# Kernel optimization log

Hardware: AMD Instinct MI355X
Metric: run time of the kernel (lower is better)

The kernel has to match this reference:

```python
import jax, jax.numpy as jnp
import numpy as np

LABEL_SIZE = 64
START = LABEL_SIZE - 2
STOP = LABEL_SIZE - 1
NEG = -10000.0


def setup_inputs() -> dict:
    key = jax.random.key(0)
    k1, k2 = jax.random.split(key)
    B, T, L = 512, 512, LABEL_SIZE
    emissions = jax.random.normal(k1, (B, T, L), dtype=jnp.float32)
    # xavier-uniform-ish init, then mask row START (nothing transitions INTO start
    # ... actually transitions[next, prev]: row START = transitions into START)
    bound = float(np.sqrt(6.0 / (L + L)))
    trans = jax.random.uniform(k2, (L, L), dtype=jnp.float32, minval=-bound, maxval=bound)
    trans = trans.at[START, :].set(NEG)   # never transition to START
    trans = trans.at[:, STOP].set(NEG)    # never transition from STOP
    return {"input": emissions, "transitions": trans}


def reference(input, transitions):
    # input: [B, T, L] emission scores; transitions[next_tag, prev_tag]: [L, L]
    B, T, L = input.shape
    init = jnp.full((B, L), NEG, dtype=input.dtype).at[:, START].set(0.0)

    def step(forward_var, emit_t):
        # forward_var: [B, L] (over prev tag); emit_t: [B, L] (over next tag)
        # scores[b, next, prev] = forward_var[b, prev] + transitions[next, prev]
        nv = jax.nn.logsumexp(forward_var[:, None, :] + transitions[None, :, :], axis=-1)
        return nv + emit_t, None

    forward_var, _ = jax.lax.scan(step, init, jnp.swapaxes(input, 0, 1))  # scan over T
    terminal = forward_var + transitions[STOP][None, :]
    return jax.nn.logsumexp(terminal, axis=-1)  # [B] log partition function
```

## Files before the change

### kernel.cpp

```cpp
#include <hip/hip_runtime.h>
#include <hip/hip_bf16.h>

#define NTAG 64
#define TLEN 512
#define START_TAG 62
#define STOP_TAG 63
#define CHUNK 32
#define HALF (TLEN / 2)

#if __has_builtin(__builtin_amdgcn_fdot2_f32_bf16)
#define USE_DOT2 1
typedef __attribute__((ext_vector_type(2))) __bf16 bfv2;
typedef __attribute__((ext_vector_type(8))) __bf16 bfv8;
#endif

__device__ __forceinline__ unsigned short f2bfu(float f) {
    __hip_bfloat16 h = __float2bfloat16(f);
    unsigned short u; __builtin_memcpy(&u, &h, 2); return u;
}
#ifdef USE_DOT2
__device__ __forceinline__ __bf16 f2bf(float f) {
    unsigned short u = f2bfu(f); __bf16 b; __builtin_memcpy(&b, &u, 2); return b;
}
#endif

__global__ __launch_bounds__(128) void crf_fwd_bwd(
    const float* __restrict__ emis,
    const float* __restrict__ trans,
    float* __restrict__ out)
{
    const int b    = blockIdx.x;
    const int tid  = threadIdx.x;
    const int lane = tid & 63;
    const int w    = tid >> 6;

    __shared__ float lds[2 * 2 * CHUNK * NTAG];
#ifdef USE_DOT2
    __shared__ __align__(16) unsigned short xbf[2][NTAG];
    unsigned short* xs = xbf[w];
#else
    __shared__ __align__(16) float xf32[2][NTAG];
    float* xs = xf32[w];
#endif
    __shared__ float shv[2][NTAG];

    const float L2E = 1.4426950408889634f;
    const float LN2 = 0.6931471805599453f;

#ifdef USE_DOT2
    bfv2 Epk[NTAG / 2];
    #pragma unroll
    for (int k2 = 0; k2 < NTAG / 2; ++k2) {
        float e0, e1;
        if (w == 0) {
            e0 = exp2f(trans[lane * NTAG + 2 * k2]     * L2E);
            e1 = exp2f(trans[lane * NTAG + 2 * k2 + 1] * L2E);
        } else {
            e0 = exp2f(trans[(2 * k2) * NTAG + lane]     * L2E);
            e1 = exp2f(trans[(2 * k2 + 1) * NTAG + lane] * L2E);
        }
        bfv2 p; p[0] = f2bf(e0); p[1] = f2bf(e1);
        Epk[k2] = p;
    }
#else
    float E[NTAG];
    #pragma unroll
    for (int k = 0; k < NTAG; ++k)
        E[k] = exp2f(((w == 0) ? trans[lane * NTAG + k]
                               : trans[k * NTAG + lane]) * L2E);
#endif

    const float* eb = emis + (size_t)b * TLEN * NTAG;

    float4 r0, r1, r2, r3, r4, r5, r6, r7;
    #define LOAD_CHUNK(baseT)                                        \
        do {                                                         \
            const float4* gp = (const float4*)(eb + (baseT) * NTAG); \
            r0 = gp[0 * 64 + lane]; r1 = gp[1 * 64 + lane];          \
            r2 = gp[2 * 64 + lane]; r3 = gp[3 * 64 + lane];          \
            r4 = gp[4 * 64 + lane]; r5 = gp[5 * 64 + lane];          \
            r6 = gp[6 * 64 + lane]; r7 = gp[7 * 64 + lane];          \
        } while (0)
    #define EXP4(v) make_float4(exp2f((v).x * L2E), exp2f((v).y * L2E), \
                                exp2f((v).z * L2E), exp2f((v).w * L2E))
    #define STORE_CHUNK_EXP(bufp)                                    \
        do {                                                         \
            float4* b4 = (float4*)(bufp);                            \
            b4[0 * 64 + lane] = EXP4(r0); b4[1 * 64 + lane] = EXP4(r1); \
            b4[2 * 64 + lane] = EXP4(r2); b4[3 * 64 + lane] = EXP4(r3); \
            b4[4 * 64 + lane] = EXP4(r4); b4[5 * 64 + lane] = EXP4(r5); \
            b4[6 * 64 + lane] = EXP4(r6); b4[7 * 64 + lane] = EXP4(r7); \
        } while (0)

#ifdef USE_DOT2
    #define PAIR(X, i) __builtin_shufflevector(X, X, 2 * (i), 2 * (i) + 1)
    #define DOTQ(acc, X, base)                                                     \
        acc = __builtin_amdgcn_fdot2_f32_bf16(Epk[(base) + 0], PAIR(X, 0), acc, false); \
        acc = __builtin_amdgcn_fdot2_f32_bf16(Epk[(base) + 1], PAIR(X, 1), acc, false); \
        acc = __builtin_amdgcn_fdot2_f32_bf16(Epk[(base) + 2], PAIR(X, 2), acc, false); \
        acc = __builtin_amdgcn_fdot2_f32_bf16(Epk[(base) + 3], PAIR(X, 3), acc, false);
    #define MATVEC_REF(ssum, e_)                                     \
        do {                                                         \
            const bfv8* xq_ = (const bfv8*)xs;                       \
            bfv8 X0 = xq_[0], X1 = xq_[1], X2 = xq_[2], X3 = xq_[3]; \
            bfv8 X4 = xq_[4], X5 = xq_[5], X6 = xq_[6], X7 = xq_[7]; \
            unsigned short ru_;                                      \
            { __bf16 rb_ = X0[0]; __builtin_memcpy(&ru_, &rb_, 2); } \
            int ef_ = (int)((ru_ >> 7) & 0xffu);                     \
            e_ = (ef_ == 0) ? 0 : ef_ - 127;                         \
            float a0 = 0.f, a1 = 0.f, a2 = 0.f, a3 = 0.f;            \
            DOTQ(a0, X0, 0)  DOTQ(a1, X1, 4)                         \
            DOTQ(a2, X2, 8)  DOTQ(a3, X3, 12)                        \
            DOTQ(a0, X4, 16) DOTQ(a1, X5, 20)                        \
            DOTQ(a2, X6, 24) DOTQ(a3, X7, 28)                        \
            ssum = (a0 + a1) + (a2 + a3);                            \
        } while (0)
    #define WRITE_STATE(v) (xs[lane] = f2bfu(v))
#else
    #define MATVEC_REF(ssum, e_)                                     \
        do {                                                         \
            const float4* xq_ = (const float4*)xs;                   \
            float4 xv_[16];                                          \
            _Pragma("unroll")                                        \
            for (int j = 0; j < 16; ++j) xv_[j] = xq_[j];            \
            int ef_ = (int)((__float_as_uint(xv_[0].x) >> 23) & 0xffu); \
            e_ = (ef_ == 0) ? 0 : ef_ - 127;                         \
            float a0=0.f,a1=0.f,a2=0.f,a3=0.f;                       \
            float a4=0.f,a5=0.f,a6=0.f,a7=0.f;                       \
            _Pragma("unroll")                                        \
            for (int j = 0; j < 16; j += 2) {                        \
                a0 = fmaf(xv_[j].x,     E[4*j + 0], a0);             \
                a1 = fmaf(xv_[j].y,     E[4*j + 1], a1);             \
                a2 = fmaf(xv_[j].z,     E[4*j + 2], a2);             \
                a3 = fmaf(xv_[j].w,     E[4*j + 3], a3);             \
                a4 = fmaf(xv_[j + 1].x, E[4*j + 4], a4);             \
                a5 = fmaf(xv_[j + 1].y, E[4*j + 5], a5);             \
                a6 = fmaf(xv_[j + 1].z, E[4*j + 6], a6);             \
                a7 = fmaf(xv_[j + 1].w, E[4*j + 7], a7);             \
            }                                                        \
            ssum = ((a0 + a1) + (a2 + a3)) + ((a4 + a5) + (a6 + a7)); \
        } while (0)
    #define WRITE_STATE(v) (xs[lane] = (v))
#endif

    #define STEP(buf, s)                                             \
        do {                                                         \
            float em_ = (buf)[(s) * NTAG + lane];                    \
            float ssum_; int e_;                                     \
            MATVEC_REF(ssum_, e_);                                   \
            off += e_;                                               \
            float rs_ = __uint_as_float((unsigned)(127 - e_) << 23); \
            x = ssum_ * em_ * rs_;                                   \
            WRITE_STATE(x);                                          \
        } while (0)

    float x = 0.0f;
    int   off = 0;

    if (w == 0) {
        WRITE_STATE(lane == START_TAG ? 1.0f : 0.0f);

        LOAD_CHUNK(0);
        #pragma clang loop unroll(disable)
        for (int ci = 0; ci < 8; ++ci) {
            float* buf = &lds[(ci & 1) * (CHUNK * NTAG)];
            STORE_CHUNK_EXP(buf);
            if (ci < 7) LOAD_CHUNK((ci + 1) * CHUNK);

            #pragma clang loop unroll_count(4)
            for (int s = 0; s < CHUNK; ++s) STEP(buf, s);
        }
    } else {
        float Sv = exp2f(trans[STOP_TAG * NTAG + lane] * L2E);

        LOAD_CHUNK(HALF + 7 * CHUNK);
        #pragma clang loop unroll(disable)
        for (int i = 0; i < 8; ++i) {
            float* buf = &lds[(2 + (i & 1)) * (CHUNK * NTAG)];
            STORE_CHUNK_EXP(buf);
            if (i < 7) LOAD_CHUNK(HALF + (6 - i) * CHUNK);

            int s0 = CHUNK - 1;
            if (i == 0) {
                WRITE_STATE(Sv * buf[(CHUNK - 1) * NTAG + lane]);
                s0 = CHUNK - 2;
            }
            #pragma clang loop unroll_count(4)
            for (int s = s0; s >= 0; --s) STEP(buf, s);
        }
        {
            float ssum_; int e_;
            MATVEC_REF(ssum_, e_);
            off += e_;
            x = ssum_ * __uint_as_float((unsigned)(127 - e_) << 23);
        }
    }

    shv[w][lane] = log2f(x) + (float)off;
    __syncthreads();

    if (w == 0) {
        float v = shv[0][lane] + shv[1][lane];
        float m = v;
        #pragma unroll
        for (int d = 1; d < 64; d <<= 1) m = fmaxf(m, __shfl_xor(m, d, 64));
        float e = exp2f(v - m);
        #pragma unroll
        for (int d = 1; d < 64; d <<= 1) e += __shfl_xor(e, d, 64);
        if (lane == 0) out[b] = LN2 * (m + log2f(e));
    }
}

extern "C" void kernel_launch(void* const* d_in, const int* in_sizes, int n_in,
                              void* d_out, int out_size, void* d_ws, size_t ws_size,
                              hipStream_t stream) {
    const float* emis  = (const float*)d_in[0];
    const float* trans = (const float*)d_in[1];
    float* out = (float*)d_out;
    (void)in_sizes; (void)n_in; (void)out_size; (void)d_ws; (void)ws_size;
    crf_fwd_bwd<<<512, 128, 0, stream>>>(emis, trans, out);
}
```

Before: 145.5 us.

## Batch 16 sequences per block and run CRF recurrence on MFMA bf16

Switches from one sequence per block with per-lane bf16 dot2 matvecs to 16 sequences per block. The exp-transition matrix times the 16-column state matrix is computed with 16x16x32 bf16 MFMA instructions. Emissions are prefetched straight from global memory into registers four steps ahead instead of being staged through LDS, and rescaling uses a per-column max exponent. The forward and backward halves are still split across the two waves. The grid shrinks from 512 to 32 blocks, so far fewer CUs are busy, and each step's latency now depends on the MFMA-to-VALU dependency chain.

```diff
diff --git a/kernel.cpp b/kernel.cpp
--- a/kernel.cpp
+++ b/kernel.cpp
@@ -1,214 +1,215 @@
 #include <hip/hip_runtime.h>
-#include <hip/hip_bf16.h>
 
 #define NTAG 64
 #define TLEN 512
 #define START_TAG 62
 #define STOP_TAG 63
-#define CHUNK 32
-#define HALF (TLEN / 2)
-
-#if __has_builtin(__builtin_amdgcn_fdot2_f32_bf16)
-#define USE_DOT2 1
-typedef __attribute__((ext_vector_type(2))) __bf16 bfv2;
-typedef __attribute__((ext_vector_type(8))) __bf16 bfv8;
+#define NB 16
+
+typedef __attribute__((ext_vector_type(4))) float    f32x4;
+typedef __attribute__((ext_vector_type(8))) short    s16x8;
+typedef __attribute__((ext_vector_type(2))) unsigned u32x2;
+typedef __attribute__((ext_vector_type(4))) unsigned u32x4;
+
+#if __has_builtin(__builtin_amdgcn_exp2f)
+#define EXP2(x) __builtin_amdgcn_exp2f(x)
+#else
+#define EXP2(x) exp2f(x)
 #endif
 
-__device__ __forceinline__ unsigned short f2bfu(float f) {
-    __hip_bfloat16 h = __float2bfloat16(f);
-    unsigned short u; __builtin_memcpy(&u, &h, 2); return u;
-}
-#ifdef USE_DOT2
-__device__ __forceinline__ __bf16 f2bf(float f) {
-    unsigned short u = f2bfu(f); __bf16 b; __builtin_memcpy(&b, &u, 2); return b;
-}
-#endif
+__device__ __forceinline__ unsigned cvtpk_bf16(float lo, float hi) {
+    unsigned r;
+    asm("v_cvt_pk_bf16_f32 %0, %1, %2" : "=v"(r) : "v"(lo), "v"(hi));
+    return r;
+}
+
+__device__ __forceinline__ f32x4 mfma32(s16x8 a, s16x8 b, f32x4 c) {
+    return __builtin_amdgcn_mfma_f32_16x16x32_bf16(a, b, c, 0, 0, 0);
+}
 
 __global__ __launch_bounds__(128) void crf_fwd_bwd(
     const float* __restrict__ emis,
     const float* __restrict__ trans,
     float* __restrict__ out)
 {
-    const int b    = blockIdx.x;
+    const int tile = blockIdx.x;
     const int tid  = threadIdx.x;
     const int lane = tid & 63;
     const int w    = tid >> 6;
-
-    __shared__ float lds[2 * 2 * CHUNK * NTAG];
-#ifdef USE_DOT2
-    __shared__ __align__(16) unsigned short xbf[2][NTAG];
-    unsigned short* xs = xbf[w];
-#else
-    __shared__ __align__(16) float xf32[2][NTAG];
-    float* xs = xf32[w];
-#endif
-    __shared__ float shv[2][NTAG];
+    const int c    = lane & 15;
+    const int g    = lane >> 4;
+    const int b0   = tile * NB;
 
     const float L2E = 1.4426950408889634f;
     const float LN2 = 0.6931471805599453f;
 
-#ifdef USE_DOT2
-    bfv2 Epk[NTAG / 2];
+    __shared__ float fy[64][17];
+    __shared__ int   offb_sh[16];
+
+    s16x8 Af[4][2];
     #pragma unroll
-    for (int k2 = 0; k2 < NTAG / 2; ++k2) {
-        float e0, e1;
-        if (w == 0) {
-            e0 = exp2f(trans[lane * NTAG + 2 * k2]     * L2E);
-            e1 = exp2f(trans[lane * NTAG + 2 * k2 + 1] * L2E);
-        } else {
-            e0 = exp2f(trans[(2 * k2) * NTAG + lane]     * L2E);
-            e1 = exp2f(trans[(2 * k2 + 1) * NTAG + lane] * L2E);
-        }
-        bfv2 p; p[0] = f2bf(e0); p[1] = f2bf(e1);
-        Epk[k2] = p;
+    for (int m = 0; m < 4; ++m) {
+        #pragma unroll
+        for (int kt = 0; kt < 2; ++kt) {
+            float ev[8];
+            #pragma unroll
+            for (int jj = 0; jj < 8; ++jj) {
+                const int r = 16 * m + c;
+                const int k = 32 * kt + 16 * (jj >> 2) + 4 * g + (jj & 3);
+                const float tv = (w == 0) ? trans[r * NTAG + k]
+                                          : trans[k * NTAG + r];
+                ev[jj] = EXP2(tv * L2E);
+            }
+            u32x4 p;
+            p[0] = cvtpk_bf16(ev[0], ev[1]);
+            p[1] = cvtpk_bf16(ev[2], ev[3]);
+            p[2] = cvtpk_bf16(ev[4], ev[5]);
+            p[3] = cvtpk_bf16(ev[6], ev[7]);
+            Af[m][kt] = __builtin_bit_cast(s16x8, p);
+        }
     }
-#else
-    float E[NTAG];
-    #pragma unroll
-    for (int k = 0; k < NTAG; ++k)
-        E[k] = exp2f(((w == 0) ? trans[lane * NTAG + k]
-                               : trans[k * NTAG + lane]) * L2E);
-#endif
-
-    const float* eb = emis + (size_t)b * TLEN * NTAG;
-
-    float4 r0, r1, r2, r3, r4, r5, r6, r7;
-    #define LOAD_CHUNK(baseT)                                        \
-        do {                                                         \
-            const float4* gp = (const float4*)(eb + (baseT) * NTAG); \
-            r0 = gp[0 * 64 + lane]; r1 = gp[1 * 64 + lane];          \
-            r2 = gp[2 * 64 + lane]; r3 = gp[3 * 64 + lane];          \
-            r4 = gp[4 * 64 + lane]; r5 = gp[5 * 64 + lane];          \
-            r6 = gp[6 * 64 + lane]; r7 = gp[7 * 64 + lane];          \
-        } while (0)
-    #define EXP4(v) make_float4(exp2f((v).x * L2E), exp2f((v).y * L2E), \
-                                exp2f((v).z * L2E), exp2f((v).w * L2E))
-    #define STORE_CHUNK_EXP(bufp)                                    \
-        do {                                                         \
-            float4* b4 = (float4*)(bufp);                            \
-            b4[0 * 64 + lane] = EXP4(r0); b4[1 * 64 + lane] = EXP4(r1); \
-            b4[2 * 64 + lane] = EXP4(r2); b4[3 * 64 + lane] = EXP4(r3); \
-            b4[4 * 64 + lane] = EXP4(r4); b4[5 * 64 + lane] = EXP4(r5); \
-            b4[6 * 64 + lane] = EXP4(r6); b4[7 * 64 + lane] = EXP4(r7); \
-        } while (0)
-
-#ifdef USE_DOT2
-    #define PAIR(X, i) __builtin_shufflevector(X, X, 2 * (i), 2 * (i) + 1)
-    #define DOTQ(acc, X, base)                                                     \
-        acc = __builtin_amdgcn_fdot2_f32_bf16(Epk[(base) + 0], PAIR(X, 0), acc, false); \
-        acc = __builtin_amdgcn_fdot2_f32_bf16(Epk[(base) + 1], PAIR(X, 1), acc, false); \
-        acc = __builtin_amdgcn_fdot2_f32_bf16(Epk[(base) + 2], PAIR(X, 2), acc, false); \
-        acc = __builtin_amdgcn_fdot2_f32_bf16(Epk[(base) + 3], PAIR(X, 3), acc, false);
-    #define MATVEC_REF(ssum, e_)                                     \
-        do {                                                         \
-            const bfv8* xq_ = (const bfv8*)xs;                       \
-            bfv8 X0 = xq_[0], X1 = xq_[1], X2 = xq_[2], X3 = xq_[3]; \
-            bfv8 X4 = xq_[4], X5 = xq_[5], X6 = xq_[6], X7 = xq_[7]; \
-            unsigned short ru_;                                      \
-            { __bf16 rb_ = X0[0]; __builtin_memcpy(&ru_, &rb_, 2); } \
-            int ef_ = (int)((ru_ >> 7) & 0xffu);                     \
-            e_ = (ef_ == 0) ? 0 : ef_ - 127;                         \
-            float a0 = 0.f, a1 = 0.f, a2 = 0.f, a3 = 0.f;            \
-            DOTQ(a0, X0, 0)  DOTQ(a1, X1, 4)                         \
-            DOTQ(a2, X2, 8)  DOTQ(a3, X3, 12)                        \
-            DOTQ(a0, X4, 16) DOTQ(a1, X5, 20)                        \
-            DOTQ(a2, X6, 24) DOTQ(a3, X7, 28)                        \
-            ssum = (a0 + a1) + (a2 + a3);                            \
-        } while (0)
-    #define WRITE_STATE(v) (xs[lane] = f2bfu(v))
-#else
-    #define MATVEC_REF(ssum, e_)                                     \
-        do {                                                         \
-            const float4* xq_ = (const float4*)xs;                   \
-            float4 xv_[16];                                          \
-            _Pragma("unroll")                                        \
-            for (int j = 0; j < 16; ++j) xv_[j] = xq_[j];            \
-            int ef_ = (int)((__float_as_uint(xv_[0].x) >> 23) & 0xffu); \
-            e_ = (ef_ == 0) ? 0 : ef_ - 127;                         \
-            float a0=0.f,a1=0.f,a2=0.f,a3=0.f;                       \
-            float a4=0.f,a5=0.f,a6=0.f,a7=0.f;                       \
-            _Pragma("unroll")                                        \
-            for (int j = 0; j < 16; j += 2) {                        \
-                a0 = fmaf(xv_[j].x,     E[4*j + 0], a0);             \
-                a1 = fmaf(xv_[j].y,     E[4*j + 1], a1);             \
-                a2 = fmaf(xv_[j].z,     E[4*j + 2], a2);             \
-                a3 = fmaf(xv_[j].w,     E[4*j + 3], a3);             \
-                a4 = fmaf(xv_[j + 1].x, E[4*j + 4], a4);             \
-                a5 = fmaf(xv_[j + 1].y, E[4*j + 5], a5);             \
-                a6 = fmaf(xv_[j + 1].z, E[4*j + 6], a6);             \
-                a7 = fmaf(xv_[j + 1].w, E[4*j + 7], a7);             \
-            }                                                        \
-            ssum = ((a0 + a1) + (a2 + a3)) + ((a4 + a5) + (a6 + a7)); \
-        } while (0)
-    #define WRITE_STATE(v) (xs[lane] = (v))
-#endif
-
-    #define STEP(buf, s)                                             \
-        do {                                                         \
-            float em_ = (buf)[(s) * NTAG + lane];                    \
-            float ssum_; int e_;                                     \
-            MATVEC_REF(ssum_, e_);                                   \
-            off += e_;                                               \
-            float rs_ = __uint_as_float((unsigned)(127 - e_) << 23); \
-            x = ssum_ * em_ * rs_;                                   \
-            WRITE_STATE(x);                                          \
-        } while (0)
-
-    float x = 0.0f;
-    int   off = 0;
+
+    const float* ebase = emis + (size_t)(b0 + c) * (TLEN * NTAG);
+
+    u32x2  Bf[4];
+    f32x4  ym[4];
+    f32x4  wq[4][4];
+    int    off  = 0;
+    int    eref = 0;
+
+    #define PREF(slot, t) do {                                         \
+        const float* _p = ebase + (t) * NTAG + 4 * g;                  \
+        wq[slot][0] = *(const f32x4*)(_p +  0);                        \
+        wq[slot][1] = *(const f32x4*)(_p + 16);                        \
+        wq[slot][2] = *(const f32x4*)(_p + 32);                        \
+        wq[slot][3] = *(const f32x4*)(_p + 48);                        \
+    } while (0)
+
+    #define BCAT(i) __builtin_bit_cast(s16x8,                          \
+        (u32x4){Bf[2*(i)].x, Bf[2*(i)].y, Bf[2*(i)+1].x, Bf[2*(i)+1].y})
+
+    #define MFMA_ALL() do {                                            \
+        s16x8 B0 = BCAT(0), B1 = BCAT(1);                              \
+        f32x4 a0 = {0.f,0.f,0.f,0.f}, a1 = a0, a2 = a0, a3 = a0;       \
+        a0 = mfma32(Af[0][0], B0, a0);                                 \
+        a1 = mfma32(Af[1][0], B0, a1);                                 \
+        a2 = mfma32(Af[2][0], B0, a2);                                 \
+        a3 = mfma32(Af[3][0], B0, a3);                                 \
+        a0 = mfma32(Af[0][1], B1, a0);                                 \
+        a1 = mfma32(Af[1][1], B1, a1);                                 \
+        a2 = mfma32(Af[2][1], B1, a2);                                 \
+        a3 = mfma32(Af[3][1], B1, a3);                                 \
+        ym[0] = a0; ym[1] = a1; ym[2] = a2; ym[3] = a3;                \
+    } while (0)
+
+    #define COLMAX_UPDATE(mxv) do {                                    \
+        float _m = (mxv);                                              \
+        _m = fmaxf(_m, __shfl_xor(_m, 16, 64));                        \
+        _m = fmaxf(_m, __shfl_xor(_m, 32, 64));                        \
+        const int _ef = (int)((__float_as_uint(_m) >> 23) & 0xffu);    \
+        eref = (_ef == 0 || _ef == 0xff) ? 0 : _ef - 127;              \
+    } while (0)
+
+    #define STEP_W(slot) do {                                          \
+        const float fne = (float)(-eref);                              \
+        off += eref;                                                   \
+        MFMA_ALL();                                                    \
+        float mx = 0.f;                                                \
+        _Pragma("unroll")                                              \
+        for (int m = 0; m < 4; ++m) {                                  \
+            _Pragma("unroll")                                          \
+            for (int j = 0; j < 4; ++j) {                              \
+                ym[m][j] *= EXP2(fmaf(wq[slot][m][j], L2E, fne));      \
+                mx = fmaxf(mx, ym[m][j]);                              \
+            }                                                          \
+            Bf[m].x = cvtpk_bf16(ym[m][0], ym[m][1]);                  \
+            Bf[m].y = cvtpk_bf16(ym[m][2], ym[m][3]);                  \
+        }                                                              \
+        COLMAX_UPDATE(mx);                                             \
+    } while (0)
+
+    #define STEP_BARE() do {                                           \
+        off += eref;                                                   \
+        const float rs = __uint_as_float((unsigned)(127 - eref) << 23);\
+        MFMA_ALL();                                                    \
+        _Pragma("unroll")                                              \
+        for (int m = 0; m < 4; ++m) ym[m] = ym[m] * rs;                \
+    } while (0)
 
     if (w == 0) {
-        WRITE_STATE(lane == START_TAG ? 1.0f : 0.0f);
-
-        LOAD_CHUNK(0);
+        Bf[0].x = 0u; Bf[0].y = 0u; Bf[1] = Bf[0]; Bf[2] = Bf[0];
+        Bf[3].x = 0u; Bf[3].y = (g == 3) ? 0x3f80u : 0u;
+        eref = 0;
+
+        PREF(0, 0); PREF(1, 1); PREF(2, 2); PREF(3, 3);
         #pragma clang loop unroll(disable)
-        for (int ci = 0; ci < 8; ++ci) {
-            float* buf = &lds[(ci & 1) * (CHUNK * NTAG)];
-            STORE_CHUNK_EXP(buf);
-            if (ci < 7) LOAD_CHUNK((ci + 1) * CHUNK);
-
-            #pragma clang loop unroll_count(4)
-            for (int s = 0; s < CHUNK; ++s) STEP(buf, s);
-        }
+        for (int it = 0; it < 63; ++it) {
+            const int t = it * 4;
+            STEP_W(0); PREF(0, t + 4);
+            STEP_W(1); PREF(1, t + 5);
+            STEP_W(2); PREF(2, t + 6);
+            STEP_W(3); PREF(3, t + 7);
+        }
+        STEP_W(0); STEP_W(1); STEP_W(2); STEP_W(3);
     } else {
-        float Sv = exp2f(trans[STOP_TAG * NTAG + lane] * L2E);
-
-        LOAD_CHUNK(HALF + 7 * CHUNK);
+        float smx = 0.f;
+        #pragma unroll
+        for (int m = 0; m < 4; ++m) {
+            const float* _p = ebase + 511 * NTAG + 16 * m + 4 * g;
+            f32x4 wv = *(const f32x4*)_p;
+            float v[4];
+            #pragma unroll
+            for (int j = 0; j < 4; ++j) {
+                const int r = 16 * m + 4 * g + j;
+                v[j] = EXP2((trans[STOP_TAG * NTAG + r] + wv[j]) * L2E);
+                smx = fmaxf(smx, v[j]);
+            }
+            Bf[m].x = cvtpk_bf16(v[0], v[1]);
+            Bf[m].y = cvtpk_bf16(v[2], v[3]);
+        }
+        COLMAX_UPDATE(smx);
+
+        PREF(0, 510); PREF(1, 509); PREF(2, 508); PREF(3, 507);
         #pragma clang loop unroll(disable)
-        for (int i = 0; i < 8; ++i) {
-            float* buf = &lds[(2 + (i & 1)) * (CHUNK * NTAG)];
-            STORE_CHUNK_EXP(buf);
-            if (i < 7) LOAD_CHUNK(HALF + (6 - i) * CHUNK);
-
-            int s0 = CHUNK - 1;
-            if (i == 0) {
-                WRITE_STATE(Sv * buf[(CHUNK - 1) * NTAG + lane]);
-                s0 = CHUNK - 2;
-            }
-            #pragma clang loop unroll_count(4)
-            for (int s = s0; s >= 0; --s) STEP(buf, s);
-        }
-        {
-            float ssum_; int e_;
-            MATVEC_REF(ssum_, e_);
-            off += e_;
-            x = ssum_ * __uint_as_float((unsigned)(127 - e_) << 23);
-        }
+        for (int it = 0; it < 63; ++it) {
+            const int t = 510 - it * 4;
+            STEP_W(0); PREF(0, t - 4);
+            STEP_W(1); PREF(1, t - 5);
+            STEP_W(2); PREF(2, t - 6);
+            STEP_W(3); PREF(3, t - 7);
+        }
+        STEP_W(0); STEP_W(1); STEP_W(2);
+        STEP_BARE();
+
+        #pragma unroll
+        for (int m = 0; m < 4; ++m)
+            #pragma unroll
+            for (int j = 0; j < 4; ++j)
+                fy[lane][4 * m + j] = ym[m][j];
+        if (lane < 16) offb_sh[lane] = off;
     }
 
-    shv[w][lane] = log2f(x) + (float)off;
     __syncthreads();
 
     if (w == 0) {
-        float v = shv[0][lane] + shv[1][lane];
-        float m = v;
-        #pragma unroll
-        for (int d = 1; d < 64; d <<= 1) m = fmaxf(m, __shfl_xor(m, d, 64));
-        float e = exp2f(v - m);
-        #pragma unroll
-        for (int d = 1; d < 64; d <<= 1) e += __shfl_xor(e, d, 64);
-        if (lane == 0) out[b] = LN2 * (m + log2f(e));
+        float p = 0.f;
+        #pragma unroll
+        for (int m = 0; m < 4; ++m)
+            #pragma unroll
+            for (int j = 0; j < 4; ++j)
+                p = fmaf(ym[m][j], fy[lane][4 * m + j], p);
+        p += __shfl_xor(p, 16, 64);
+        p += __shfl_xor(p, 32, 64);
+        if (lane < 16)
+            out[b0 + lane] = LN2 * (log2f(p) + (float)(off + offb_sh[lane]));
     }
+
+    #undef PREF
+    #undef BCAT
+    #undef MFMA_ALL
+    #undef COLMAX_UPDATE
+    #undef STEP_W
+    #undef STEP_BARE
 }
 
 extern "C" void kernel_launch(void* const* d_in, const int* in_sizes, int n_in,
@@ -218,5 +219,5 @@
     const float* trans = (const float*)d_in[1];
     float* out = (float*)d_out;
     (void)in_sizes; (void)n_in; (void)out_size; (void)d_ws; (void)ws_size;
-    crf_fwd_bwd<<<512, 128, 0, stream>>>(emis, trans, out);
-}
+    crf_fwd_bwd<<<512 / NB, 128, 0, stream>>>(emis, trans, out);
+}
```

New measurement: 155.8 us. 1.07x slower.
